# Kernel optimization log

Hardware: AMD Instinct MI355X
Metric: run time of the kernel (lower is better)

Reference implementation:

```python
import jax, jax.numpy as jnp
import numpy as np

E = 800000
N = 50000
D = 128
SLOPE = 0.2


def setup_inputs() -> dict:
    key = jax.random.key(0)
    ks = jax.random.split(key, 8)
    M = jax.random.normal(ks[0], (E, D), dtype=jnp.float32)
    dest = jax.random.randint(ks[1], (E,), 0, N, dtype=jnp.int32)
    rev_index = jax.random.randint(ks[2], (E,), 0, E, dtype=jnp.int32)
    s = 1.0 / np.sqrt(D)
    W0 = jax.random.uniform(ks[3], (D, D), jnp.float32, -s, s)
    b0 = jax.random.uniform(ks[4], (D,), jnp.float32, -s, s)
    W1 = jax.random.uniform(ks[5], (D, D), jnp.float32, -s, s)
    b1 = jax.random.uniform(ks[6], (D,), jnp.float32, -s, s)
    sa = 1.0 / np.sqrt(D)
    a_w = jax.random.uniform(ks[7], (1, D), jnp.float32, -sa, sa)
    a_b = jnp.zeros((1,), jnp.float32)
    return {"M": M, "dest": dest, "rev_index": rev_index, "dim_size": N,
            "W0": W0, "b0": b0, "W1": W1, "b1": b1, "a_w": a_w, "a_b": a_b}


def reference(M, dest, rev_index, dim_size, W0, b0, W1, b1, a_w, a_b):
    # Z = LeakyReLU(W_0(M) + W_1(M[rev_index]))  -> [E, D]
    Z = jax.nn.leaky_relu(M @ W0.T + b0 + M[rev_index] @ W1.T + b1, negative_slope=SLOPE)
    # scores = a(Z) -> [E, 1]; segment softmax over dest
    s = (Z @ a_w.T + a_b)[:, 0]  # [E]
    smax = jax.ops.segment_max(s, dest, num_segments=dim_size)  # [N]
    e = jnp.exp(s - smax[dest])
    denom = jax.ops.segment_sum(e, dest, num_segments=dim_size)  # [N]
    alpha = (e / denom[dest])[:, None]  # [E, 1]
    out = jax.ops.segment_sum(alpha * M, dest, num_segments=dim_size)  # [N, D]
    return out, alpha
```

## Files before the change

### kernel.cpp

```cpp
#include <hip/hip_runtime.h>


#define SLOPE 0.2f
constexpr int E = 800000;
constexpr int N = 50000;
constexpr int D = 128;
constexpr int TILE_E = 64;
constexpr int NTILES = E / TILE_E;
constexpr int LDA = 264;
constexpr int MAXDEG = 64;
constexpr int SGRID = 512;

typedef __attribute__((ext_vector_type(8))) _Float16 f16x8;
typedef __attribute__((ext_vector_type(4))) _Float16 f16x4;
typedef __attribute__((ext_vector_type(2))) _Float16 f16x2;
typedef __attribute__((ext_vector_type(4))) float f32x4;

__global__ void convert_w(const float* __restrict__ W0, const float* __restrict__ W1,
                          _Float16* __restrict__ Wh) {
    int i = blockIdx.x * blockDim.x + threadIdx.x;
    if (i >= D * 256) return;
    int d = i >> 8, k = i & 255;
    float v = (k < 128) ? W0[d * 128 + k] : W1[d * 128 + (k - 128)];
    Wh[i] = (_Float16)v;
}

__global__ __launch_bounds__(256) void convert_m(const float* __restrict__ M,
                                                 _Float16* __restrict__ Mh) {
    const int total = E * D / 4;
    for (int u = blockIdx.x * blockDim.x + threadIdx.x; u < total;
         u += gridDim.x * blockDim.x) {
        float4 v = ((const float4*)M)[u];
        f16x4 h = { (_Float16)v.x, (_Float16)v.y, (_Float16)v.z, (_Float16)v.w };
        ((f16x4*)Mh)[u] = h;
    }
}

__global__ void bucket_build(const int* __restrict__ dest, int* __restrict__ cnt,
                             int* __restrict__ bucket) {
    int e = blockIdx.x * blockDim.x + threadIdx.x;
    if (e >= E) return;
    int n = dest[e];
    int pos = atomicAdd(&cnt[n], 1);
    if (pos < MAXDEG) bucket[n * MAXDEG + pos] = e;
}

__global__ __launch_bounds__(512, 4) void score_kernel(
    const _Float16* __restrict__ Mh, const int* __restrict__ dest,
    const int* __restrict__ rev, const _Float16* __restrict__ Wh,
    const float* __restrict__ b0, const float* __restrict__ b1,
    const float* __restrict__ a_w, const float* __restrict__ a_b,
    float* __restrict__ pbuf, float* __restrict__ denom)
{
    __shared__ _Float16 Alds[TILE_E * LDA];
    __shared__ float red[4][TILE_E];

    const int t = threadIdx.x;
    const int w = t >> 6;
    const int lane = t & 63;
    const int lo = lane & 15, hi = lane >> 4;
    const int er = (w & 1) * 32;
    const int dr = (w >> 1) * 32;

    f16x8 b[2][8];
#pragma unroll
    for (int j = 0; j < 2; ++j) {
        int d = dr + j * 16 + lo;
#pragma unroll
        for (int ks = 0; ks < 8; ++ks)
            b[j][ks] = *(const f16x8*)(Wh + d * 256 + ks * 32 + hi * 8);
    }
    float bs[2], aw[2];
#pragma unroll
    for (int j = 0; j < 2; ++j) {
        int d = dr + j * 16 + lo;
        bs[j] = b0[d] + b1[d];
        aw[j] = a_w[d];
    }
    const float ab = a_b[0];

    const int c16 = t & 15;
    const int r16 = t >> 4;

    for (int tile = blockIdx.x; tile < NTILES; tile += SGRID) {
        const int eb = tile * TILE_E;
        __syncthreads();

#pragma unroll
        for (int q = 0; q < 2; ++q) {
            int r = r16 + q * 32;
            int rv = rev[eb + r];
            f16x8 hs = ((const f16x8*)(Mh + (size_t)(eb + r) * D))[c16];
            f16x8 hr = ((const f16x8*)(Mh + (size_t)rv * D))[c16];
            *(f16x8*)(Alds + r * LDA + c16 * 8) = hs;
            *(f16x8*)(Alds + r * LDA + 128 + c16 * 8) = hr;
        }
        __syncthreads();

        f32x4 zero = {0.f, 0.f, 0.f, 0.f};
        f32x4 acc[2][2];
#pragma unroll
        for (int i = 0; i < 2; ++i)
#pragma unroll
            for (int j = 0; j < 2; ++j) acc[i][j] = zero;

#pragma unroll
        for (int ks = 0; ks < 8; ++ks) {
            f16x8 a[2];
#pragma unroll
            for (int i = 0; i < 2; ++i)
                a[i] = *(const f16x8*)(Alds + (er + i * 16 + lo) * LDA + ks * 32 + hi * 8);
#pragma unroll
            for (int i = 0; i < 2; ++i)
#pragma unroll
                for (int j = 0; j < 2; ++j)
                    acc[i][j] = __builtin_amdgcn_mfma_f32_16x16x32_f16(a[i], b[j][ks], acc[i][j], 0, 0, 0);
        }

#pragma unroll
        for (int i = 0; i < 2; ++i) {
#pragma unroll
            for (int r = 0; r < 4; ++r) {
                float v = 0.f;
#pragma unroll
                for (int j = 0; j < 2; ++j) {
                    float x = acc[i][j][r] + bs[j];
                    x = (x > 0.f) ? x : SLOPE * x;
                    v += aw[j] * x;
                }
                v += __shfl_xor(v, 1);
                v += __shfl_xor(v, 2);
                v += __shfl_xor(v, 4);
                v += __shfl_xor(v, 8);
                if (lo == 0) red[w >> 1][er + i * 16 + hi * 4 + r] = v;
            }
        }
        __syncthreads();

        if (t < TILE_E) {
            int e = eb + t;
            float s = red[0][t] + red[1][t] + red[2][t] + red[3][t] + ab;
            float p = __expf(s);
            pbuf[e] = p;
            atomicAdd(&denom[dest[e]], p);
        }
    }
}

__global__ __launch_bounds__(256) void gather_kernel(
    const _Float16* __restrict__ Mh, float* __restrict__ alpha,
    const float* __restrict__ denom,
    const int* __restrict__ cnt, const int* __restrict__ bucket,
    float* __restrict__ out)
{
    const int n = blockIdx.x * 4 + (threadIdx.x >> 6);
    const int lane = threadIdx.x & 63;
    int c = cnt[n];
    c = (c > MAXDEG) ? MAXDEG : c;
    const float dn = denom[n];
    int e = 0; float a = 0.f;
    if (lane < c) {
        e = bucket[n * MAXDEG + lane];
        a = alpha[e] / dn;
        alpha[e] = a;
    }
    float2 acc = {0.f, 0.f};
    int i = 0;
    for (; i + 4 <= c; i += 4) {
        int e0 = __builtin_amdgcn_readlane(e, i + 0);
        int e1 = __builtin_amdgcn_readlane(e, i + 1);
        int e2 = __builtin_amdgcn_readlane(e, i + 2);
        int e3 = __builtin_amdgcn_readlane(e, i + 3);
        float a0 = __uint_as_float(__builtin_amdgcn_readlane(__float_as_uint(a), i + 0));
        float a1 = __uint_as_float(__builtin_amdgcn_readlane(__float_as_uint(a), i + 1));
        float a2 = __uint_as_float(__builtin_amdgcn_readlane(__float_as_uint(a), i + 2));
        float a3 = __uint_as_float(__builtin_amdgcn_readlane(__float_as_uint(a), i + 3));
        f16x2 v0 = ((const f16x2*)(Mh + (size_t)e0 * D))[lane];
        f16x2 v1 = ((const f16x2*)(Mh + (size_t)e1 * D))[lane];
        f16x2 v2 = ((const f16x2*)(Mh + (size_t)e2 * D))[lane];
        f16x2 v3 = ((const f16x2*)(Mh + (size_t)e3 * D))[lane];
        acc.x = fmaf(a0, (float)v0.x, acc.x); acc.y = fmaf(a0, (float)v0.y, acc.y);
        acc.x = fmaf(a1, (float)v1.x, acc.x); acc.y = fmaf(a1, (float)v1.y, acc.y);
        acc.x = fmaf(a2, (float)v2.x, acc.x); acc.y = fmaf(a2, (float)v2.y, acc.y);
        acc.x = fmaf(a3, (float)v3.x, acc.x); acc.y = fmaf(a3, (float)v3.y, acc.y);
    }
    for (; i < c; ++i) {
        int   ei = __builtin_amdgcn_readlane(e, i);
        float ai = __uint_as_float(__builtin_amdgcn_readlane(__float_as_uint(a), i));
        f16x2 v = ((const f16x2*)(Mh + (size_t)ei * D))[lane];
        acc.x = fmaf(ai, (float)v.x, acc.x);
        acc.y = fmaf(ai, (float)v.y, acc.y);
    }
    ((float2*)(out + (size_t)n * D))[lane] = acc;
}

extern "C" void kernel_launch(void* const* d_in, const int* in_sizes, int n_in,
                              void* d_out, int out_size, void* d_ws, size_t ws_size,
                              hipStream_t stream) {
    const float* M   = (const float*)d_in[0];
    const int*   dst = (const int*)d_in[1];
    const int*   rev = (const int*)d_in[2];
    const float* W0  = (const float*)d_in[4];
    const float* b0  = (const float*)d_in[5];
    const float* W1  = (const float*)d_in[6];
    const float* b1  = (const float*)d_in[7];
    const float* a_w = (const float*)d_in[8];
    const float* a_b = (const float*)d_in[9];

    float* out   = (float*)d_out;
    float* alpha = out + (size_t)N * D;

    float*     denom  = (float*)d_ws;
    int*       cnt    = (int*)(denom + N);
    _Float16*  Wh     = (_Float16*)(cnt + N);
    _Float16*  Mh     = Wh + D * 256;
    int*       bucket = (int*)(Mh + (size_t)E * D);

    hipMemsetAsync(denom, 0, (size_t)2 * N * sizeof(float), stream);

    convert_w<<<128, 256, 0, stream>>>(W0, W1, Wh);
    convert_m<<<4096, 256, 0, stream>>>(M, Mh);
    bucket_build<<<(E + 255) / 256, 256, 0, stream>>>(dst, cnt, bucket);
    score_kernel<<<SGRID, 512, 0, stream>>>(Mh, dst, rev, Wh, b0, b1, a_w, a_b,
                                            alpha, denom);
    gather_kernel<<<N / 4, 256, 0, stream>>>(Mh, alpha, denom, cnt, bucket, out);
}
```

Measured before the change: 800.1 us.

## Fuse score, segment softmax and gather into one per-destination-node kernel

Replaces the separate fp16 conversion pass over M, the tiled score kernel with atomic denominators, and the gather kernel with one kernel launched per destination node. Each block loads the node's bucketed edges and their reverse rows from fp32 M, converts them to fp16 in LDS, runs the MFMA score GEMM, does the segment softmax in-wave, and reuses the LDS rows for the weighted sum. This removes the full Mh write and re-read, the denom atomics and a launch. The cost is MFMA tiles padded for variable degree, a 50000-block grid, and the weighted sum now accumulating from fp16 copies held in LDS. It also subtracts the segment max inside softmax.

```diff
diff --git a/kernel.cpp b/kernel.cpp
--- a/kernel.cpp
+++ b/kernel.cpp
@@ -5,15 +5,11 @@
 constexpr int E = 800000;
 constexpr int N = 50000;
 constexpr int D = 128;
-constexpr int TILE_E = 64;
-constexpr int NTILES = E / TILE_E;
 constexpr int LDA = 264;
 constexpr int MAXDEG = 64;
-constexpr int SGRID = 512;
 
 typedef __attribute__((ext_vector_type(8))) _Float16 f16x8;
 typedef __attribute__((ext_vector_type(4))) _Float16 f16x4;
-typedef __attribute__((ext_vector_type(2))) _Float16 f16x2;
 typedef __attribute__((ext_vector_type(4))) float f32x4;
 
 __global__ void convert_w(const float* __restrict__ W0, const float* __restrict__ W1,
@@ -25,17 +21,6 @@
     Wh[i] = (_Float16)v;
 }
 
-__global__ __launch_bounds__(256) void convert_m(const float* __restrict__ M,
-                                                 _Float16* __restrict__ Mh) {
-    const int total = E * D / 4;
-    for (int u = blockIdx.x * blockDim.x + threadIdx.x; u < total;
-         u += gridDim.x * blockDim.x) {
-        float4 v = ((const float4*)M)[u];
-        f16x4 h = { (_Float16)v.x, (_Float16)v.y, (_Float16)v.z, (_Float16)v.w };
-        ((f16x4*)Mh)[u] = h;
-    }
-}
-
 __global__ void bucket_build(const int* __restrict__ dest, int* __restrict__ cnt,
                              int* __restrict__ bucket) {
     int e = blockIdx.x * blockDim.x + threadIdx.x;
@@ -45,22 +30,29 @@
     if (pos < MAXDEG) bucket[n * MAXDEG + pos] = e;
 }
 
-__global__ __launch_bounds__(512, 4) void score_kernel(
-    const _Float16* __restrict__ Mh, const int* __restrict__ dest,
-    const int* __restrict__ rev, const _Float16* __restrict__ Wh,
+__global__ __launch_bounds__(256, 4) void fused_kernel(
+    const float* __restrict__ M, const int* __restrict__ rev,
+    const _Float16* __restrict__ Wh,
     const float* __restrict__ b0, const float* __restrict__ b1,
     const float* __restrict__ a_w, const float* __restrict__ a_b,
-    float* __restrict__ pbuf, float* __restrict__ denom)
+    const int* __restrict__ cnt, const int* __restrict__ bucket,
+    float* __restrict__ out, float* __restrict__ alpha)
 {
-    __shared__ _Float16 Alds[TILE_E * LDA];
-    __shared__ float red[4][TILE_E];
+    __shared__ _Float16 Alds[MAXDEG * LDA];
+    __shared__ float red[4][MAXDEG];
+    __shared__ float alf[MAXDEG];
+    __shared__ int ebL[MAXDEG];
+    __shared__ int rvL[MAXDEG];
 
+    const int n = blockIdx.x;
     const int t = threadIdx.x;
     const int w = t >> 6;
     const int lane = t & 63;
     const int lo = lane & 15, hi = lane >> 4;
-    const int er = (w & 1) * 32;
-    const int dr = (w >> 1) * 32;
+    const int dr = w * 32;
+
+    int c = cnt[n];
+    c = (c > MAXDEG) ? MAXDEG : c;
 
     f16x8 b[2][8];
 #pragma unroll
@@ -79,52 +71,58 @@
     }
     const float ab = a_b[0];
 
-    const int c16 = t & 15;
-    const int r16 = t >> 4;
+    if (t < MAXDEG) {
+        int e = 0, rv = 0;
+        if (t < c) { e = bucket[n * MAXDEG + t]; rv = rev[e]; }
+        ebL[t] = e; rvL[t] = rv;
+    }
+    __syncthreads();
 
-    for (int tile = blockIdx.x; tile < NTILES; tile += SGRID) {
-        const int eb = tile * TILE_E;
-        __syncthreads();
+    const int col = t & 31;
+    const int rr  = t >> 5;
+    for (int i0 = 0; i0 < c; i0 += 8) {
+        int i = i0 + rr;
+        if (i < c) {
+            const float4 v = ((const float4*)(M + (size_t)ebL[i] * D))[col];
+            const float4 u = ((const float4*)(M + (size_t)rvL[i] * D))[col];
+            f16x4 hv = { (_Float16)v.x, (_Float16)v.y, (_Float16)v.z, (_Float16)v.w };
+            f16x4 hu = { (_Float16)u.x, (_Float16)u.y, (_Float16)u.z, (_Float16)u.w };
+            *(f16x4*)(Alds + i * LDA + col * 4) = hv;
+            *(f16x4*)(Alds + i * LDA + 128 + col * 4) = hu;
+        }
+    }
+    __syncthreads();
 
-#pragma unroll
-        for (int q = 0; q < 2; ++q) {
-            int r = r16 + q * 32;
-            int rv = rev[eb + r];
-            f16x8 hs = ((const f16x8*)(Mh + (size_t)(eb + r) * D))[c16];
-            f16x8 hr = ((const f16x8*)(Mh + (size_t)rv * D))[c16];
-            *(f16x8*)(Alds + r * LDA + c16 * 8) = hs;
-            *(f16x8*)(Alds + r * LDA + 128 + c16 * 8) = hr;
-        }
-        __syncthreads();
-
+    const int nb = (c + 15) >> 4;
+    for (int ib0 = 0; ib0 < nb; ib0 += 2) {
+        const int nbi = (nb - ib0 < 2) ? (nb - ib0) : 2;
+        const int r1 = (ib0 + 1 < nb) ? (ib0 + 1) : ib0;
         f32x4 zero = {0.f, 0.f, 0.f, 0.f};
         f32x4 acc[2][2];
 #pragma unroll
-        for (int i = 0; i < 2; ++i)
+        for (int ii = 0; ii < 2; ++ii)
 #pragma unroll
-            for (int j = 0; j < 2; ++j) acc[i][j] = zero;
+            for (int j = 0; j < 2; ++j) acc[ii][j] = zero;
 
 #pragma unroll
         for (int ks = 0; ks < 8; ++ks) {
             f16x8 a[2];
+            a[0] = *(const f16x8*)(Alds + (ib0 * 16 + lo) * LDA + ks * 32 + hi * 8);
+            a[1] = *(const f16x8*)(Alds + (r1  * 16 + lo) * LDA + ks * 32 + hi * 8);
 #pragma unroll
-            for (int i = 0; i < 2; ++i)
-                a[i] = *(const f16x8*)(Alds + (er + i * 16 + lo) * LDA + ks * 32 + hi * 8);
-#pragma unroll
-            for (int i = 0; i < 2; ++i)
+            for (int ii = 0; ii < 2; ++ii)
 #pragma unroll
                 for (int j = 0; j < 2; ++j)
-                    acc[i][j] = __builtin_amdgcn_mfma_f32_16x16x32_f16(a[i], b[j][ks], acc[i][j], 0, 0, 0);
+                    acc[ii][j] = __builtin_amdgcn_mfma_f32_16x16x32_f16(a[ii], b[j][ks], acc[ii][j], 0, 0, 0);
         }
 
-#pragma unroll
-        for (int i = 0; i < 2; ++i) {
+        for (int ii = 0; ii < nbi; ++ii) {
 #pragma unroll
             for (int r = 0; r < 4; ++r) {
                 float v = 0.f;
 #pragma unroll
                 for (int j = 0; j < 2; ++j) {
-                    float x = acc[i][j][r] + bs[j];
+                    float x = acc[ii][j][r] + bs[j];
                     x = (x > 0.f) ? x : SLOPE * x;
                     v += aw[j] * x;
                 }
@@ -132,66 +130,36 @@
                 v += __shfl_xor(v, 2);
                 v += __shfl_xor(v, 4);
                 v += __shfl_xor(v, 8);
-                if (lo == 0) red[w >> 1][er + i * 16 + hi * 4 + r] = v;
+                if (lo == 0) red[w][(ib0 + ii) * 16 + hi * 4 + r] = v;
             }
         }
-        __syncthreads();
+    }
+    __syncthreads();
 
-        if (t < TILE_E) {
-            int e = eb + t;
-            float s = red[0][t] + red[1][t] + red[2][t] + red[3][t] + ab;
-            float p = __expf(s);
-            pbuf[e] = p;
-            atomicAdd(&denom[dest[e]], p);
-        }
+    if (t < MAXDEG) {
+        float s = (t < c) ? (red[0][t] + red[1][t] + red[2][t] + red[3][t] + ab) : -3.0e38f;
+        float m = s;
+#pragma unroll
+        for (int off = 1; off < 64; off <<= 1) m = fmaxf(m, __shfl_xor(m, off));
+        float p = (t < c) ? __expf(s - m) : 0.f;
+        float dsum = p;
+#pragma unroll
+        for (int off = 1; off < 64; off <<= 1) dsum += __shfl_xor(dsum, off);
+        float al = (t < c) ? (p / dsum) : 0.f;
+        alf[t] = al;
+        if (t < c) alpha[ebL[t]] = al;
     }
-}
+    __syncthreads();
 
-__global__ __launch_bounds__(256) void gather_kernel(
-    const _Float16* __restrict__ Mh, float* __restrict__ alpha,
-    const float* __restrict__ denom,
-    const int* __restrict__ cnt, const int* __restrict__ bucket,
-    float* __restrict__ out)
-{
-    const int n = blockIdx.x * 4 + (threadIdx.x >> 6);
-    const int lane = threadIdx.x & 63;
-    int c = cnt[n];
-    c = (c > MAXDEG) ? MAXDEG : c;
-    const float dn = denom[n];
-    int e = 0; float a = 0.f;
-    if (lane < c) {
-        e = bucket[n * MAXDEG + lane];
-        a = alpha[e] / dn;
-        alpha[e] = a;
+    {
+        const int cl = lane & 31;
+        const int half = lane >> 5;
+        float a0 = 0.f;
+        for (int i = half; i < c; i += 2)
+            a0 = fmaf(alf[i], (float)Alds[i * LDA + dr + cl], a0);
+        a0 += __shfl_xor(a0, 32);
+        if (half == 0) out[(size_t)n * D + dr + cl] = a0;
     }
-    float2 acc = {0.f, 0.f};
-    int i = 0;
-    for (; i + 4 <= c; i += 4) {
-        int e0 = __builtin_amdgcn_readlane(e, i + 0);
-        int e1 = __builtin_amdgcn_readlane(e, i + 1);
-        int e2 = __builtin_amdgcn_readlane(e, i + 2);
-        int e3 = __builtin_amdgcn_readlane(e, i + 3);
-        float a0 = __uint_as_float(__builtin_amdgcn_readlane(__float_as_uint(a), i + 0));
-        float a1 = __uint_as_float(__builtin_amdgcn_readlane(__float_as_uint(a), i + 1));
-        float a2 = __uint_as_float(__builtin_amdgcn_readlane(__float_as_uint(a), i + 2));
-        float a3 = __uint_as_float(__builtin_amdgcn_readlane(__float_as_uint(a), i + 3));
-        f16x2 v0 = ((const f16x2*)(Mh + (size_t)e0 * D))[lane];
-        f16x2 v1 = ((const f16x2*)(Mh + (size_t)e1 * D))[lane];
-        f16x2 v2 = ((const f16x2*)(Mh + (size_t)e2 * D))[lane];
-        f16x2 v3 = ((const f16x2*)(Mh + (size_t)e3 * D))[lane];
-        acc.x = fmaf(a0, (float)v0.x, acc.x); acc.y = fmaf(a0, (float)v0.y, acc.y);
-        acc.x = fmaf(a1, (float)v1.x, acc.x); acc.y = fmaf(a1, (float)v1.y, acc.y);
-        acc.x = fmaf(a2, (float)v2.x, acc.x); acc.y = fmaf(a2, (float)v2.y, acc.y);
-        acc.x = fmaf(a3, (float)v3.x, acc.x); acc.y = fmaf(a3, (float)v3.y, acc.y);
-    }
-    for (; i < c; ++i) {
-        int   ei = __builtin_amdgcn_readlane(e, i);
-        float ai = __uint_as_float(__builtin_amdgcn_readlane(__float_as_uint(a), i));
-        f16x2 v = ((const f16x2*)(Mh + (size_t)ei * D))[lane];
-        acc.x = fmaf(ai, (float)v.x, acc.x);
-        acc.y = fmaf(ai, (float)v.y, acc.y);
-    }
-    ((float2*)(out + (size_t)n * D))[lane] = acc;
 }
 
 extern "C" void kernel_launch(void* const* d_in, const int* in_sizes, int n_in,
@@ -210,18 +178,14 @@
     float* out   = (float*)d_out;
     float* alpha = out + (size_t)N * D;
 
-    float*     denom  = (float*)d_ws;
-    int*       cnt    = (int*)(denom + N);
+    int*       cnt    = (int*)d_ws;
     _Float16*  Wh     = (_Float16*)(cnt + N);
-    _Float16*  Mh     = Wh + D * 256;
-    int*       bucket = (int*)(Mh + (size_t)E * D);
+    int*       bucket = (int*)(Wh + D * 256);
 
-    hipMemsetAsync(denom, 0, (size_t)2 * N * sizeof(float), stream);
+    hipMemsetAsync(cnt, 0, (size_t)N * sizeof(int), stream);
 
     convert_w<<<128, 256, 0, stream>>>(W0, W1, Wh);
-    convert_m<<<4096, 256, 0, stream>>>(M, Mh);
     bucket_build<<<(E + 255) / 256, 256, 0, stream>>>(dst, cnt, bucket);
-    score_kernel<<<SGRID, 512, 0, stream>>>(Mh, dst, rev, Wh, b0, b1, a_w, a_b,
-                                            alpha, denom);
-    gather_kernel<<<N / 4, 256, 0, stream>>>(Mh, alpha, denom, cnt, bucket, out);
+    fused_kernel<<<N, 256, 0, stream>>>(M, rev, Wh, b0, b1, a_w, a_b,
+                                        cnt, bucket, out, alpha);
 }
```

Result: slower. 990.9 us (+23.9%).
